# Kernel optimization log

Hardware: AMD Instinct MI355X
Metric: run time of the kernel (lower is better)

## Reference

```python
import jax, jax.numpy as jnp
import numpy as np

D_MODEL = 1024
QK_DIM = 1024
V_DIM = 1024
H = 16
TAU = 20.0
HQK = QK_DIM // H
HV = V_DIM // H
SCALE = HQK ** -0.5
SCALE_BASE = 512.0
EPS_GAMMA = 1e-8
EPS_GN = 1e-5


def _rotate_every_two(x):
    x1 = x[..., ::2]
    x2 = x[..., 1::2]
    return jnp.stack([-x2, x1], axis=-1).reshape(x.shape)


def _xpos_rotate(q, k, t):
    # q,k: (B,H,N,d); t: (B,N) continuous positions (timestamps in days)
    d = q.shape[-1]
    inv_freq = (1.0 / (10000.0 ** (np.arange(0, d, 2) / d))).astype(np.float32)  # (d/2,)
    sinusoid = t[:, None, :, None] * inv_freq  # (B,1,N,d/2)
    sin = jnp.repeat(jnp.sin(sinusoid), 2, axis=-1)  # (B,1,N,d)
    cos = jnp.repeat(jnp.cos(sinusoid), 2, axis=-1)
    scale_vec = ((np.arange(0, d, 2) + 0.4 * d) / (1.4 * d)).astype(np.float32)  # (d/2,)
    scale = jnp.repeat(scale_vec ** (t[:, None, :, None] / SCALE_BASE), 2, axis=-1)  # (B,1,N,d)
    q_rot = (q * cos + _rotate_every_two(q) * sin) * scale
    k_rot = (k * cos + _rotate_every_two(k) * sin) / scale
    return q_rot, k_rot


def setup_inputs() -> dict:
    key = jax.random.key(0)
    ks = jax.random.split(key, 6)
    B, N = 4, 1024
    X = jax.random.normal(ks[0], (B, N, D_MODEL), dtype=jnp.float32)
    # increasing timestamps in days
    timestamps = jnp.sort(jax.random.uniform(ks[1], (B, N), jnp.float32, 0.0, 100.0), axis=-1)
    W_qkv = jax.random.normal(ks[2], (D_MODEL, 2 * QK_DIM + V_DIM), dtype=jnp.float32) * 0.02
    W_gamma = jax.random.normal(ks[3], (D_MODEL, H), dtype=jnp.float32) * 0.02
    W_gated = jax.random.normal(ks[4], (D_MODEL, V_DIM), dtype=jnp.float32) * 0.02
    W_out = jax.random.normal(ks[5], (V_DIM, D_MODEL), dtype=jnp.float32) * 0.02
    return {"X": X, "timestamps": timestamps, "W_qkv": W_qkv, "W_gamma": W_gamma,
            "W_gated": W_gated, "W_out": W_out}


def reference(X, timestamps, W_qkv, W_gamma, W_gated, W_out):
    B, N, _ = X.shape
    qkv = X @ W_qkv  # (B,N,2*qk+v)
    q, k, v = jnp.split(qkv, [QK_DIM, 2 * QK_DIM], axis=-1)
    q = q.reshape(B, N, H, HQK).transpose(0, 2, 1, 3)  # (B,H,N,dk)
    k = k.reshape(B, N, H, HQK).transpose(0, 2, 1, 3)
    v = v.reshape(B, N, H, HV).transpose(0, 2, 1, 3)
    q, k = _xpos_rotate(q, k, timestamps)
    # data-dependent decay gamma in (0,1]
    gamma = jax.nn.sigmoid(X @ W_gamma) ** (1.0 / TAU)  # (B,N,H)
    log_b = jnp.cumsum(jnp.log(gamma + EPS_GAMMA), axis=1).transpose(0, 2, 1)  # (B,H,N)
    log_D = log_b[..., :, None] - log_b[..., None, :]  # (B,H,N,N)
    causal = jnp.tril(jnp.ones((N, N), dtype=bool))
    # masked_fill(-inf) then clamp[-80,0]: clip maps -inf -> -80 (matches torch)
    D = jnp.exp(jnp.clip(jnp.where(causal, log_D, -jnp.inf), -80.0, 0.0))
    attn = jnp.einsum('bhnd,bhmd->bhnm', q, k) * SCALE * D
    O = jnp.einsum('bhnm,bhmd->bhnd', attn, v)  # (B,H,N,dv)
    O = O.transpose(0, 2, 1, 3).reshape(B, N, V_DIM)
    # GroupNorm(num_groups=H, affine=False) over (channels-in-group, seq)
    g = O.reshape(B, N, H, HV)
    mu = g.mean(axis=(1, 3), keepdims=True)
    var = g.var(axis=(1, 3), keepdims=True)
    O = ((g - mu) / jnp.sqrt(var + EPS_GN)).reshape(B, N, V_DIM)
    O = jax.nn.silu(X @ W_gated) * O
    return O @ W_out
```

## Files before the change

### kernel.cpp

```cpp
#include <hip/hip_runtime.h>
#include <cstddef>
#include <cstdint>

#define NH 16
#define HD 64
#define NSEQ 1024
#define NB 4
#define DM 1024
#define SCALE 0.125f

typedef __attribute__((ext_vector_type(8))) short v8s;
typedef __attribute__((ext_vector_type(4))) float v4f;

__device__ __forceinline__ short f2bf(float x) {
    union { float f; unsigned u; } v; v.f = x;
    unsigned r = v.u + 0x7FFF + ((v.u >> 16) & 1);
    return (short)(r >> 16);
}
__device__ __forceinline__ float bf2f(short x) {
    union { unsigned u; float f; } v; v.u = ((unsigned)(unsigned short)x) << 16;
    return v.f;
}
__device__ __forceinline__ void gload16(const void* g, void* l) {
    __builtin_amdgcn_global_load_lds(
        (const __attribute__((address_space(1))) void*)g,
        (__attribute__((address_space(3))) void*)l, 16, 0, 0);
}
__device__ __forceinline__ int gswz(int r, int kbyte) {
    return (r * 64 + kbyte) ^ (((r >> 1) & 3) << 4);
}
__device__ __forceinline__ int aswz(int r, int byte) {
    return (r * 128 + byte) ^ ((r & 7) << 4);
}
#define SBAR() __builtin_amdgcn_s_barrier()
#define WAITV0() asm volatile("s_waitcnt vmcnt(0)" ::: "memory")
#define WAITV4() asm volatile("s_waitcnt vmcnt(4)" ::: "memory")
#define WAITL() asm volatile("s_waitcnt lgkmcnt(0)" ::: "memory")

__global__ __launch_bounds__(256) void convert_rows(const float* __restrict__ X,
                                                    short* __restrict__ Xb, int K) {
    const int kt = blockIdx.x, rt = blockIdx.y;
    const int t = threadIdx.x;
    const int rloc = t >> 1, kb0 = (t & 1) * 16;
    const float* src = X + (size_t)(rt * 128 + rloc) * K + kt * 32 + kb0;
    short o[16] __attribute__((aligned(16)));
#pragma unroll
    for (int j = 0; j < 16; j += 4) {
        float4 v = *(const float4*)(src + j);
        o[j] = f2bf(v.x); o[j + 1] = f2bf(v.y); o[j + 2] = f2bf(v.z); o[j + 3] = f2bf(v.w);
    }
    char* base = (char*)(Xb + ((size_t)rt * (K >> 5) + kt) * 4096);
#pragma unroll
    for (int c = 0; c < 2; ++c)
        *(v8s*)(base + gswz(rloc, kb0 * 2 + c * 16)) = *(v8s*)&o[c * 8];
}

__global__ __launch_bounds__(256) void tconv(const float* __restrict__ W,
                                             short* __restrict__ Bt,
                                             int K, int N) {
    __shared__ short lsm[32][136];
    const int ct = blockIdx.x, kt = blockIdx.y;
    const int t = threadIdx.x;
    {
        const int kk = t >> 3, nn0 = (t & 7) * 16;
        const float* src = W + (size_t)(kt * 32 + kk) * N + ct * 128 + nn0;
#pragma unroll
        for (int j = 0; j < 16; j += 4) {
            float4 v = *(const float4*)(src + j);
            lsm[kk][nn0 + j] = f2bf(v.x); lsm[kk][nn0 + j + 1] = f2bf(v.y);
            lsm[kk][nn0 + j + 2] = f2bf(v.z); lsm[kk][nn0 + j + 3] = f2bf(v.w);
        }
    }
    __syncthreads();
    const int rloc = t >> 1, kb0 = (t & 1) * 16;
    short o[16] __attribute__((aligned(16)));
#pragma unroll
    for (int j = 0; j < 16; ++j) o[j] = lsm[kb0 + j][rloc];
    char* base = (char*)(Bt + ((size_t)ct * (K >> 5) + kt) * 4096);
#pragma unroll
    for (int c = 0; c < 2; ++c)
        *(v8s*)(base + gswz(rloc, kb0 * 2 + c * 16)) = *(v8s*)&o[c * 8];
}

template<bool BF16OUT>
__global__ __launch_bounds__(256) void gemm_tt(const short* __restrict__ A,
                                               const short* __restrict__ B,
                                               void* __restrict__ C, int N) {
    __shared__ short As[4096];
    __shared__ short Bs[4096];
    const int tid = threadIdx.x;
    const int w = tid >> 6, l = tid & 63;
    const int wr = w >> 1, wc = w & 1;
    const int rt = blockIdx.y, ct = blockIdx.x;
    const char* Abase = (const char*)A + ((size_t)rt * 32) * 8192;
    const char* Bbase = (const char*)B + ((size_t)ct * 32) * 8192;

    v4f acc[4][4];
#pragma unroll
    for (int i = 0; i < 4; ++i)
#pragma unroll
        for (int j = 0; j < 4; ++j) acc[i][j] = (v4f){0.f, 0.f, 0.f, 0.f};

    for (int kt = 0; kt < 32; ++kt) {
        __syncthreads();
#pragma unroll
        for (int i = 0; i < 2; ++i) {
            const int c = w * 2 + i;
            gload16(Abase + (size_t)kt * 8192 + c * 1024 + l * 16, (char*)As + c * 1024);
            gload16(Bbase + (size_t)kt * 8192 + c * 1024 + l * 16, (char*)Bs + c * 1024);
        }
        __syncthreads();
        v8s af[4], bfr[4];
#pragma unroll
        for (int i = 0; i < 4; ++i) {
            const int ra = wr * 64 + i * 16 + (l & 15);
            af[i] = *(const v8s*)((char*)As + gswz(ra, (l >> 4) * 16));
            const int rb = wc * 64 + i * 16 + (l & 15);
            bfr[i] = *(const v8s*)((char*)Bs + gswz(rb, (l >> 4) * 16));
        }
#pragma unroll
        for (int i = 0; i < 4; ++i)
#pragma unroll
            for (int j = 0; j < 4; ++j)
                acc[i][j] = __builtin_amdgcn_mfma_f32_16x16x32_bf16(af[i], bfr[j], acc[i][j], 0, 0, 0);
    }
#pragma unroll
    for (int i = 0; i < 4; ++i)
#pragma unroll
        for (int j = 0; j < 4; ++j) {
            const int r0 = rt * 128 + wr * 64 + i * 16 + (l >> 4) * 4;
            const int cc = ct * 128 + wc * 64 + j * 16 + (l & 15);
#pragma unroll
            for (int t2 = 0; t2 < 4; ++t2) {
                if (BF16OUT) ((short*)C)[(size_t)(r0 + t2) * N + cc] = f2bf(acc[i][j][t2]);
                else         ((float*)C)[(size_t)(r0 + t2) * N + cc] = acc[i][j][t2];
            }
        }
}

__global__ __launch_bounds__(256) void gamma2(const float* __restrict__ X,
                                              const float* __restrict__ Wg,
                                              float* __restrict__ loggam) {
    __shared__ float wgs[1024 * 17];
    const int tid = threadIdx.x;
#pragma unroll
    for (int it = 0; it < 16; ++it) {
        const int idx = it * 1024 + tid * 4;
        float4 v = *(const float4*)(Wg + idx);
        const int k = idx >> 4, h0 = idx & 15;
        wgs[k * 17 + h0]     = v.x;
        wgs[k * 17 + h0 + 1] = v.y;
        wgs[k * 17 + h0 + 2] = v.z;
        wgs[k * 17 + h0 + 3] = v.w;
    }
    __syncthreads();

    const int r = tid >> 4, c = tid & 15;
    const int row = blockIdx.x * 16 + r;
    const float* xrow = X + (size_t)row * DM;
    float acc[16];
#pragma unroll
    for (int h = 0; h < 16; ++h) acc[h] = 0.0f;
#pragma unroll 4
    for (int i = 0; i < 16; ++i) {
        const int kb = i * 64 + c * 4;
        float4 xv = *(const float4*)(xrow + kb);
        const float xs[4] = {xv.x, xv.y, xv.z, xv.w};
#pragma unroll
        for (int j = 0; j < 4; ++j) {
            const float* wrow = &wgs[(kb + j) * 17];
#pragma unroll
            for (int h = 0; h < 16; ++h) acc[h] = fmaf(xs[j], wrow[h], acc[h]);
        }
    }
#pragma unroll
    for (int h = 0; h < 16; ++h) {
#pragma unroll
        for (int off = 8; off >= 1; off >>= 1)
            acc[h] += __shfl_xor(acc[h], off, 16);
    }
    const float d = acc[c];
    const float sig = 1.0f / (1.0f + expf(-d));
    const float gam = powf(sig, 1.0f / 20.0f);
    loggam[(size_t)row * NH + c] = logf(gam + 1e-8f);
}

__global__ __launch_bounds__(256) void scan_kernel(float* __restrict__ lg) {
    const int wave = threadIdx.x >> 6;
    const int lane = threadIdx.x & 63;
    const int bh = blockIdx.x * 4 + wave;
    const int b = bh >> 4, h = bh & 15;
    float* p = lg + (size_t)b * NSEQ * NH + h;
    const int n0 = lane * 16;
    float v[16];
    float s = 0.0f;
#pragma unroll
    for (int j = 0; j < 16; ++j) { v[j] = p[(size_t)(n0 + j) * NH]; s += v[j]; }
    float sc = s;
#pragma unroll
    for (int off = 1; off < 64; off <<= 1) {
        float o = __shfl_up(sc, off, 64);
        if (lane >= off) sc += o;
    }
    float acc = sc - s;
#pragma unroll
    for (int j = 0; j < 16; ++j) { acc += v[j]; p[(size_t)(n0 + j) * NH] = acc; }
}

__global__ __launch_bounds__(256) void prep(const short* __restrict__ qkvb,
                                            const float* __restrict__ ts,
                                            short* __restrict__ Qb,
                                            short* __restrict__ Kb,
                                            short* __restrict__ Vtb) {
    __shared__ short vsm[64][72];
    const int tile = blockIdx.x, bh = blockIdx.y;
    const int b = bh >> 4, h = bh & 15;
    const int t = threadIdx.x;
    const int rloc = t >> 2, d0 = (t & 3) * 16;
    const int row = b * NSEQ + tile * 64 + rloc;
    const short* src = qkvb + (size_t)row * 3072 + h * HD;
    const size_t tb = ((size_t)bh * 16 + tile) * 4096;

    float qa[16], ka[16];
    {
        v8s q0 = *(const v8s*)(src + d0), q1 = *(const v8s*)(src + d0 + 8);
        v8s k0 = *(const v8s*)(src + 1024 + d0), k1 = *(const v8s*)(src + 1024 + d0 + 8);
#pragma unroll
        for (int j = 0; j < 8; ++j) {
            qa[j] = bf2f(q0[j]); qa[j + 8] = bf2f(q1[j]);
            ka[j] = bf2f(k0[j]); ka[j + 8] = bf2f(k1[j]);
        }
    }
    const float tv = ts[row];
    short qo[16] __attribute__((aligned(16)));
    short ko[16] __attribute__((aligned(16)));
#pragma unroll
    for (int j = 0; j < 8; ++j) {
        const int i = (d0 >> 1) + j;
        const float inv_freq = exp2f(-0.4152410119f * (float)i);
        const float ang = tv * inv_freq;
        const float s = sinf(ang), c = cosf(ang);
        const float sv = ((float)(2 * i) + 25.6f) * (1.0f / 89.6f);
        const float e = log2f(sv) * tv * (1.0f / 512.0f);
        const float sc = exp2f(e) * SCALE, isc = exp2f(-e);
        qo[2 * j]     = f2bf((qa[2 * j] * c - qa[2 * j + 1] * s) * sc);
        qo[2 * j + 1] = f2bf((qa[2 * j + 1] * c + qa[2 * j] * s) * sc);
        ko[2 * j]     = f2bf((ka[2 * j] * c - ka[2 * j + 1] * s) * isc);
        ko[2 * j + 1] = f2bf((ka[2 * j + 1] * c + ka[2 * j] * s) * isc);
    }
#pragma unroll
    for (int c = 0; c < 2; ++c) {
        *(v8s*)((char*)(Qb + tb) + aswz(rloc, d0 * 2 + c * 16)) = *(v8s*)&qo[c * 8];
        *(v8s*)((char*)(Kb + tb) + aswz(rloc, d0 * 2 + c * 16)) = *(v8s*)&ko[c * 8];
    }
    {
        v8s v0 = *(const v8s*)(src + 2048 + d0), v1 = *(const v8s*)(src + 2048 + d0 + 8);
        *(short4*)&vsm[rloc][d0]      = *(short4*)&v0;
        *(short4*)&vsm[rloc][d0 + 4]  = *((short4*)&v0 + 1);
        *(short4*)&vsm[rloc][d0 + 8]  = *(short4*)&v1;
        *(short4*)&vsm[rloc][d0 + 12] = *((short4*)&v1 + 1);
    }
    __syncthreads();
    {
        const int d = t >> 2, m0 = (t & 3) * 16;
        short vt[16] __attribute__((aligned(16)));
#pragma unroll
        for (int j = 0; j < 16; ++j) vt[j] = vsm[m0 + j][d];
#pragma unroll
        for (int c = 0; c < 2; ++c)
            *(v8s*)((char*)(Vtb + tb) + aswz(d, m0 * 2 + c * 16)) = *(v8s*)&vt[c * 8];
    }
}

__global__ __launch_bounds__(256) void attn4(const short* __restrict__ Qb,
                                             const short* __restrict__ Kb,
                                             const short* __restrict__ Vtb,
                                             const float* __restrict__ logb,
                                             float* __restrict__ O,
                                             float* __restrict__ partial) {
    __shared__ short Ks[2][4096];
    __shared__ short Vts[2][4096];
    __shared__ short Ps[8192];
    __shared__ float lbAll[1024];
    __shared__ float emAll[1024];
    const int id = blockIdx.x;
    const int half = id >> 8;
    const int idx = id & 255;
    const int bh = ((idx & 7) << 3) | ((idx >> 3) & 7);
    const int qq = half == 0 ? (4 + (idx >> 6)) : (3 - (idx >> 6));
    const int b = bh >> 4, h = bh & 15;
    const int tid = threadIdx.x;
    const int w = tid >> 6, l = tid & 63;
    const int n0 = qq * 128;
    const int NT = 2 * qq + 2;

#pragma unroll
    for (int i = 0; i < 4; ++i) {
        const int c = w * 4 + i;
        gload16((const char*)Qb + ((size_t)bh * 16 + 2 * qq) * 8192 + c * 1024 + l * 16,
                (char*)Ps + c * 1024);
    }
    for (int i = tid; i < 1024; i += 256)
        lbAll[i] = logb[(size_t)(b * NSEQ + i) * NH + h];
    WAITV0(); WAITL();
    SBAR();

    const float base = lbAll[n0];
    for (int i = tid; i < NT * 64; i += 256) emAll[i] = __expf(base - lbAll[i]);
    float en[2][4];
#pragma unroll
    for (int rg = 0; rg < 2; ++rg)
#pragma unroll
        for (int t2 = 0; t2 < 4; ++t2)
            en[rg][t2] = __expf(lbAll[n0 + w * 32 + rg * 16 + (l >> 4) * 4 + t2] - base);
    v8s aq[2][2];
#pragma unroll
    for (int rg = 0; rg < 2; ++rg)
#pragma unroll
        for (int kc = 0; kc < 2; ++kc) {
            const int r = w * 32 + rg * 16 + (l & 15);
            aq[rg][kc] = *(const v8s*)((char*)Ps + (r >> 6) * 8192 +
                                       aswz(r & 63, kc * 64 + (l >> 4) * 16));
        }
    WAITL();
    SBAR();

    v4f oacc[2][4];
#pragma unroll
    for (int rg = 0; rg < 2; ++rg)
#pragma unroll
        for (int dt = 0; dt < 4; ++dt) oacc[rg][dt] = (v4f){0.f, 0.f, 0.f, 0.f};

#pragma unroll
    for (int i = 0; i < 2; ++i) {
        const int c = w * 2 + i;
        gload16((const char*)Kb + ((size_t)bh * 16 + 0) * 8192 + c * 1024 + l * 16,
                (char*)Ks + c * 1024);
        gload16((const char*)Vtb + ((size_t)bh * 16 + 0) * 8192 + c * 1024 + l * 16,
                (char*)Vts + c * 1024);
    }

    for (int t = 0; t < NT; ++t) {
        const int m0 = t * 64;
        const int buf = t & 1;
        SBAR();
        if (t + 1 < NT) {
            const int nb = (t + 1) & 1;
#pragma unroll
            for (int i = 0; i < 2; ++i) {
                const int c = w * 2 + i;
                gload16((const char*)Kb + ((size_t)bh * 16 + t + 1) * 8192 + c * 1024 + l * 16,
                        (char*)Ks + nb * 8192 + c * 1024);
                gload16((const char*)Vtb + ((size_t)bh * 16 + t + 1) * 8192 + c * 1024 + l * 16,
                        (char*)Vts + nb * 8192 + c * 1024);
            }
            WAITV4();
        } else {
            WAITV0();
        }
        SBAR();

        const bool active = (m0 <= n0 + w * 32 + 31);
        if (active) {
            const char* KsB = (const char*)Ks + buf * 8192;
            const char* VtsB = (const char*)Vts + buf * 8192;
            v4f sfr[2][4];
#pragma unroll
            for (int rg = 0; rg < 2; ++rg)
#pragma unroll
                for (int m4 = 0; m4 < 4; ++m4) sfr[rg][m4] = (v4f){0.f, 0.f, 0.f, 0.f};
#pragma unroll
            for (int m4 = 0; m4 < 4; ++m4) {
#pragma unroll
                for (int kc = 0; kc < 2; ++kc) {
                    const int m = m4 * 16 + (l & 15);
                    v8s bk = *(const v8s*)(KsB + aswz(m, kc * 64 + (l >> 4) * 16));
#pragma unroll
                    for (int rg = 0; rg < 2; ++rg)
                        sfr[rg][m4] = __builtin_amdgcn_mfma_f32_16x16x32_bf16(aq[rg][kc], bk, sfr[rg][m4], 0, 0, 0);
                }
            }
            const bool needMask = (m0 + 63) > (n0 + w * 32);
            float emv[4];
#pragma unroll
            for (int m4 = 0; m4 < 4; ++m4) emv[m4] = emAll[m0 + m4 * 16 + (l & 15)];
#pragma unroll
            for (int rg = 0; rg < 2; ++rg)
#pragma unroll
                for (int m4 = 0; m4 < 4; ++m4) {
                    const int m = m4 * 16 + (l & 15);
#pragma unroll
                    for (int t2 = 0; t2 < 4; ++t2) {
                        const int r = w * 32 + rg * 16 + (l >> 4) * 4 + t2;
                        float sval = sfr[rg][m4][t2] * en[rg][t2] * emv[m4];
                        if (needMask && (n0 + r) < (m0 + m)) sval = 0.0f;
                        *(short*)((char*)Ps + aswz(r, m * 2)) = f2bf(sval);
                    }
                }
            WAITL();
            __builtin_amdgcn_sched_barrier(0);
#pragma unroll
            for (int kc = 0; kc < 2; ++kc) {
                v8s ap[2];
#pragma unroll
                for (int rg = 0; rg < 2; ++rg) {
                    const int r = w * 32 + rg * 16 + (l & 15);
                    ap[rg] = *(const v8s*)((char*)Ps + aswz(r, kc * 64 + (l >> 4) * 16));
                }
#pragma unroll
                for (int dt = 0; dt < 4; ++dt) {
                    const int d = dt * 16 + (l & 15);
                    v8s bv = *(const v8s*)(VtsB + aswz(d, kc * 64 + (l >> 4) * 16));
#pragma unroll
                    for (int rg = 0; rg < 2; ++rg)
                        oacc[rg][dt] = __builtin_amdgcn_mfma_f32_16x16x32_bf16(ap[rg], bv, oacc[rg][dt], 0, 0, 0);
                }
            }
        }
    }
    float psum = 0.0f, pssq = 0.0f;
#pragma unroll
    for (int rg = 0; rg < 2; ++rg)
#pragma unroll
        for (int dt = 0; dt < 4; ++dt) {
            const int col = h * HD + dt * 16 + (l & 15);
            const int r0 = n0 + w * 32 + rg * 16 + (l >> 4) * 4;
#pragma unroll
            for (int t2 = 0; t2 < 4; ++t2) {
                const float v = oacc[rg][dt][t2];
                O[(size_t)(b * NSEQ + r0 + t2) * DM + col] = v;
                psum += v; pssq += v * v;
            }
        }
    __syncthreads();
    float* red = (float*)Ks;
    red[tid] = psum; red[256 + tid] = pssq;
    __syncthreads();
    for (int s = 128; s > 0; s >>= 1) {
        if (tid < s) { red[tid] += red[tid + s]; red[256 + tid] += red[256 + tid + s]; }
        __syncthreads();
    }
    if (tid == 0) {
        partial[(bh * 8 + qq) * 2]     = red[0];
        partial[(bh * 8 + qq) * 2 + 1] = red[256];
    }
}

__global__ __launch_bounds__(64) void gn_finalize(const float* __restrict__ partial,
                                                  float* __restrict__ stats) {
    const int bh = threadIdx.x;
    float s = 0.0f, q = 0.0f;
#pragma unroll
    for (int i = 0; i < 8; ++i) {
        s += partial[(bh * 8 + i) * 2];
        q += partial[(bh * 8 + i) * 2 + 1];
    }
    const float inv = 1.0f / (NSEQ * HD);
    const float mu = s * inv;
    const float var = q * inv - mu * mu;
    stats[bh * 2] = mu;
    stats[bh * 2 + 1] = rsqrtf(var + 1e-5f);
}

__global__ __launch_bounds__(256) void gate_kernel(const short* __restrict__ Gfb,
                                                   const float* __restrict__ O,
                                                   const float* __restrict__ stats,
                                                   short* __restrict__ Gb) {
    const size_t i4 = ((size_t)blockIdx.x * 256 + threadIdx.x) * 4;
    const int row = (int)(i4 >> 10);
    const int col = (int)(i4 & 1023);
    const int h = col >> 6;
    const int b = row >> 10;
    const float mu = stats[(b * NH + h) * 2];
    const float rstd = stats[(b * NH + h) * 2 + 1];
    short4 gv = *(const short4*)(Gfb + i4);
    float4 ov = *(const float4*)(O + i4);
    const float gs[4] = {bf2f(gv.x), bf2f(gv.y), bf2f(gv.z), bf2f(gv.w)};
    const float os[4] = {ov.x, ov.y, ov.z, ov.w};
    short o[4];
#pragma unroll
    for (int j = 0; j < 4; ++j) {
        const float g = gs[j];
        const float silu = g / (1.0f + __expf(-g));
        o[j] = f2bf(silu * (os[j] - mu) * rstd);
    }
    const int rt = row >> 7, rloc = row & 127;
    const int kt = col >> 5, kloc = col & 31;
    char* base = (char*)(Gb + ((size_t)rt * 32 + kt) * 4096);
    *(short4*)(base + gswz(rloc, kloc * 2)) = *(short4*)o;
}

extern "C" void kernel_launch(void* const* d_in, const int* in_sizes, int n_in,
                              void* d_out, int out_size, void* d_ws, size_t ws_size,
                              hipStream_t stream) {
    const float* X       = (const float*)d_in[0];
    const float* ts      = (const float*)d_in[1];
    const float* W_qkv   = (const float*)d_in[2];
    const float* W_gamma = (const float*)d_in[3];
    const float* W_gated = (const float*)d_in[4];
    const float* W_out   = (const float*)d_in[5];
    float* out = (float*)d_out;

    char* ws = (char*)d_ws;
    short* qkvb = (short*)ws;
    float* logb = (float*)(ws + 25165824);
    float* Oatt = (float*)(ws + 25427968);
    float* stats = (float*)(ws + 42205184);
    short* Xb   = (short*)(ws + 42205696);
    short* Wtq  = (short*)(ws + 50594304);
    short* Wtg  = (short*)(ws + 56885760);
    short* Wto  = (short*)(ws + 58982912);
    short* Qb   = (short*)(ws + 61080064);
    short* Kb   = (short*)(ws + 69468672);
    short* Vtb  = (short*)(ws + 77857280);
    short* Gfb  = qkvb;
    short* Gb   = Xb;
    float* partial = (float*)Wtq;

    convert_rows<<<dim3(32, 32), 256, 0, stream>>>(X, Xb, 1024);
    tconv<<<dim3(24, 32), 256, 0, stream>>>(W_qkv, Wtq, 1024, 3072);
    tconv<<<dim3(8, 32), 256, 0, stream>>>(W_gated, Wtg, 1024, 1024);
    tconv<<<dim3(8, 32), 256, 0, stream>>>(W_out, Wto, 1024, 1024);

    gemm_tt<true><<<dim3(24, 32), 256, 0, stream>>>(Xb, Wtq, qkvb, 3072);
    gamma2<<<256, 256, 0, stream>>>(X, W_gamma, logb);
    scan_kernel<<<16, 256, 0, stream>>>(logb);
    prep<<<dim3(16, 64), 256, 0, stream>>>(qkvb, ts, Qb, Kb, Vtb);
    attn4<<<512, 256, 0, stream>>>(Qb, Kb, Vtb, logb, Oatt, partial);
    gn_finalize<<<1, 64, 0, stream>>>(partial, stats);
    gemm_tt<true><<<dim3(8, 32), 256, 0, stream>>>(Xb, Wtg, Gfb, 1024);
    gate_kernel<<<4096, 256, 0, stream>>>(Gfb, Oatt, stats, Gb);
    gemm_tt<false><<<dim3(8, 32), 256, 0, stream>>>(Gb, Wto, out, 1024);
}
```

Measured before the change: 168.3 us.

## Fuse gating epilogue into gated GEMM and transpose attention MFMA outputs

Merges the SiLU gating and group-norm application into the epilogue of the gated GEMM, which removes the separate gate kernel and the bf16 round trip of the gate activations. The scan now writes log-decay in a transposed per-(batch,head) layout so attention loads it contiguously. In attention, the MFMA operands are swapped so each lane holds a row with consecutive columns, which allows vectorized P stores and float4 O stores. The new GEMM epilogue does scattered scalar reads of O and swizzled 2-byte writes, which may be less efficient than the old dedicated kernel.

```diff
diff --git a/kernel.cpp b/kernel.cpp
--- a/kernel.cpp
+++ b/kernel.cpp
@@ -82,10 +82,12 @@
         *(v8s*)(base + gswz(rloc, kb0 * 2 + c * 16)) = *(v8s*)&o[c * 8];
 }
 
-template<bool BF16OUT>
+template<int MODE>
 __global__ __launch_bounds__(256) void gemm_tt(const short* __restrict__ A,
                                                const short* __restrict__ B,
-                                               void* __restrict__ C, int N) {
+                                               void* __restrict__ C, int N,
+                                               const float* __restrict__ O,
+                                               const float* __restrict__ stats) {
     __shared__ short As[4096];
     __shared__ short Bs[4096];
     const int tid = threadIdx.x;
@@ -124,6 +126,12 @@
             for (int j = 0; j < 4; ++j)
                 acc[i][j] = __builtin_amdgcn_mfma_f32_16x16x32_bf16(af[i], bfr[j], acc[i][j], 0, 0, 0);
     }
+    float mu = 0.f, rstd = 0.f;
+    if (MODE == 2) {
+        const int hh = ct * 2 + wc;
+        mu   = stats[((rt >> 3) * NH + hh) * 2];
+        rstd = stats[((rt >> 3) * NH + hh) * 2 + 1];
+    }
 #pragma unroll
     for (int i = 0; i < 4; ++i)
 #pragma unroll
@@ -132,8 +140,18 @@
             const int cc = ct * 128 + wc * 64 + j * 16 + (l & 15);
 #pragma unroll
             for (int t2 = 0; t2 < 4; ++t2) {
-                if (BF16OUT) ((short*)C)[(size_t)(r0 + t2) * N + cc] = f2bf(acc[i][j][t2]);
-                else         ((float*)C)[(size_t)(r0 + t2) * N + cc] = acc[i][j][t2];
+                if (MODE == 1) ((short*)C)[(size_t)(r0 + t2) * N + cc] = f2bf(acc[i][j][t2]);
+                else if (MODE == 0) ((float*)C)[(size_t)(r0 + t2) * N + cc] = acc[i][j][t2];
+                else {
+                    const int row = r0 + t2;
+                    const float g = acc[i][j][t2];
+                    const float silu = g / (1.0f + __expf(-g));
+                    const float ov = O[(size_t)row * DM + cc];
+                    const float val = silu * (ov - mu) * rstd;
+                    const int rloc = row - rt * 128;
+                    char* base = (char*)((short*)C + ((size_t)rt * 32 + (cc >> 5)) * 4096);
+                    *(short*)(base + gswz(rloc, (cc & 31) * 2)) = f2bf(val);
+                }
             }
         }
 }
@@ -185,12 +203,13 @@
     loggam[(size_t)row * NH + c] = logf(gam + 1e-8f);
 }
 
-__global__ __launch_bounds__(256) void scan_kernel(float* __restrict__ lg) {
+__global__ __launch_bounds__(256) void scan_kernel(const float* __restrict__ lg,
+                                                   float* __restrict__ lgT) {
     const int wave = threadIdx.x >> 6;
     const int lane = threadIdx.x & 63;
     const int bh = blockIdx.x * 4 + wave;
     const int b = bh >> 4, h = bh & 15;
-    float* p = lg + (size_t)b * NSEQ * NH + h;
+    const float* p = lg + (size_t)b * NSEQ * NH + h;
     const int n0 = lane * 16;
     float v[16];
     float s = 0.0f;
@@ -203,8 +222,9 @@
         if (lane >= off) sc += o;
     }
     float acc = sc - s;
-#pragma unroll
-    for (int j = 0; j < 16; ++j) { acc += v[j]; p[(size_t)(n0 + j) * NH] = acc; }
+    float* q = lgT + (size_t)bh * NSEQ + n0;
+#pragma unroll
+    for (int j = 0; j < 16; ++j) { acc += v[j]; q[j] = acc; }
 }
 
 __global__ __launch_bounds__(256) void prep(const short* __restrict__ qkvb,
@@ -272,10 +292,10 @@
     }
 }
 
-__global__ __launch_bounds__(256) void attn4(const short* __restrict__ Qb,
+__global__ __launch_bounds__(256) void attn5(const short* __restrict__ Qb,
                                              const short* __restrict__ Kb,
                                              const short* __restrict__ Vtb,
-                                             const float* __restrict__ logb,
+                                             const float* __restrict__ logbT,
                                              float* __restrict__ O,
                                              float* __restrict__ partial) {
     __shared__ short Ks[2][4096];
@@ -301,18 +321,16 @@
                 (char*)Ps + c * 1024);
     }
     for (int i = tid; i < 1024; i += 256)
-        lbAll[i] = logb[(size_t)(b * NSEQ + i) * NH + h];
+        lbAll[i] = logbT[(size_t)bh * NSEQ + i];
     WAITV0(); WAITL();
     SBAR();
 
     const float base = lbAll[n0];
     for (int i = tid; i < NT * 64; i += 256) emAll[i] = __expf(base - lbAll[i]);
-    float en[2][4];
+    float en[2];
 #pragma unroll
     for (int rg = 0; rg < 2; ++rg)
-#pragma unroll
-        for (int t2 = 0; t2 < 4; ++t2)
-            en[rg][t2] = __expf(lbAll[n0 + w * 32 + rg * 16 + (l >> 4) * 4 + t2] - base);
+        en[rg] = __expf(lbAll[n0 + w * 32 + rg * 16 + (l & 15)] - base);
     v8s aq[2][2];
 #pragma unroll
     for (int rg = 0; rg < 2; ++rg)
@@ -377,26 +395,29 @@
                     v8s bk = *(const v8s*)(KsB + aswz(m, kc * 64 + (l >> 4) * 16));
 #pragma unroll
                     for (int rg = 0; rg < 2; ++rg)
-                        sfr[rg][m4] = __builtin_amdgcn_mfma_f32_16x16x32_bf16(aq[rg][kc], bk, sfr[rg][m4], 0, 0, 0);
+                        sfr[rg][m4] = __builtin_amdgcn_mfma_f32_16x16x32_bf16(bk, aq[rg][kc], sfr[rg][m4], 0, 0, 0);
                 }
             }
             const bool needMask = (m0 + 63) > (n0 + w * 32);
-            float emv[4];
-#pragma unroll
-            for (int m4 = 0; m4 < 4; ++m4) emv[m4] = emAll[m0 + m4 * 16 + (l & 15)];
-#pragma unroll
-            for (int rg = 0; rg < 2; ++rg)
+#pragma unroll
+            for (int rg = 0; rg < 2; ++rg) {
+                const int r = w * 32 + rg * 16 + (l & 15);
+                const float enr = en[rg];
 #pragma unroll
                 for (int m4 = 0; m4 < 4; ++m4) {
-                    const int m = m4 * 16 + (l & 15);
+                    const int mbase = m0 + m4 * 16 + (l >> 4) * 4;
+                    float4 emv = *(const float4*)&emAll[mbase];
+                    const float ems[4] = {emv.x, emv.y, emv.z, emv.w};
+                    union { short s[4]; uint2 u; } pk;
 #pragma unroll
                     for (int t2 = 0; t2 < 4; ++t2) {
-                        const int r = w * 32 + rg * 16 + (l >> 4) * 4 + t2;
-                        float sval = sfr[rg][m4][t2] * en[rg][t2] * emv[m4];
-                        if (needMask && (n0 + r) < (m0 + m)) sval = 0.0f;
-                        *(short*)((char*)Ps + aswz(r, m * 2)) = f2bf(sval);
+                        float sval = sfr[rg][m4][t2] * enr * ems[t2];
+                        if (needMask && (n0 + r) < (mbase + t2)) sval = 0.0f;
+                        pk.s[t2] = f2bf(sval);
                     }
+                    *(uint2*)((char*)Ps + aswz(r, (m4 * 16 + (l >> 4) * 4) * 2)) = pk.u;
                 }
+            }
             WAITL();
             __builtin_amdgcn_sched_barrier(0);
 #pragma unroll
@@ -413,25 +434,23 @@
                     v8s bv = *(const v8s*)(VtsB + aswz(d, kc * 64 + (l >> 4) * 16));
 #pragma unroll
                     for (int rg = 0; rg < 2; ++rg)
-                        oacc[rg][dt] = __builtin_amdgcn_mfma_f32_16x16x32_bf16(ap[rg], bv, oacc[rg][dt], 0, 0, 0);
+                        oacc[rg][dt] = __builtin_amdgcn_mfma_f32_16x16x32_bf16(bv, ap[rg], oacc[rg][dt], 0, 0, 0);
                 }
             }
         }
     }
     float psum = 0.0f, pssq = 0.0f;
 #pragma unroll
-    for (int rg = 0; rg < 2; ++rg)
+    for (int rg = 0; rg < 2; ++rg) {
+        const int row = n0 + w * 32 + rg * 16 + (l & 15);
 #pragma unroll
         for (int dt = 0; dt < 4; ++dt) {
-            const int col = h * HD + dt * 16 + (l & 15);
-            const int r0 = n0 + w * 32 + rg * 16 + (l >> 4) * 4;
-#pragma unroll
-            for (int t2 = 0; t2 < 4; ++t2) {
-                const float v = oacc[rg][dt][t2];
-                O[(size_t)(b * NSEQ + r0 + t2) * DM + col] = v;
-                psum += v; pssq += v * v;
-            }
-        }
+            const float4 v = {oacc[rg][dt][0], oacc[rg][dt][1], oacc[rg][dt][2], oacc[rg][dt][3]};
+            *(float4*)(O + (size_t)(b * NSEQ + row) * DM + h * HD + dt * 16 + (l >> 4) * 4) = v;
+            psum += v.x + v.y + v.z + v.w;
+            pssq += v.x * v.x + v.y * v.y + v.z * v.z + v.w * v.w;
+        }
+    }
     __syncthreads();
     float* red = (float*)Ks;
     red[tid] = psum; red[256 + tid] = pssq;
@@ -460,34 +479,6 @@
     const float var = q * inv - mu * mu;
     stats[bh * 2] = mu;
     stats[bh * 2 + 1] = rsqrtf(var + 1e-5f);
-}
-
-__global__ __launch_bounds__(256) void gate_kernel(const short* __restrict__ Gfb,
-                                                   const float* __restrict__ O,
-                                                   const float* __restrict__ stats,
-                                                   short* __restrict__ Gb) {
-    const size_t i4 = ((size_t)blockIdx.x * 256 + threadIdx.x) * 4;
-    const int row = (int)(i4 >> 10);
-    const int col = (int)(i4 & 1023);
-    const int h = col >> 6;
-    const int b = row >> 10;
-    const float mu = stats[(b * NH + h) * 2];
-    const float rstd = stats[(b * NH + h) * 2 + 1];
-    short4 gv = *(const short4*)(Gfb + i4);
-    float4 ov = *(const float4*)(O + i4);
-    const float gs[4] = {bf2f(gv.x), bf2f(gv.y), bf2f(gv.z), bf2f(gv.w)};
-    const float os[4] = {ov.x, ov.y, ov.z, ov.w};
-    short o[4];
-#pragma unroll
-    for (int j = 0; j < 4; ++j) {
-        const float g = gs[j];
-        const float silu = g / (1.0f + __expf(-g));
-        o[j] = f2bf(silu * (os[j] - mu) * rstd);
-    }
-    const int rt = row >> 7, rloc = row & 127;
-    const int kt = col >> 5, kloc = col & 31;
-    char* base = (char*)(Gb + ((size_t)rt * 32 + kt) * 4096);
-    *(short4*)(base + gswz(rloc, kloc * 2)) = *(short4*)o;
 }
 
 extern "C" void kernel_launch(void* const* d_in, const int* in_sizes, int n_in,
@@ -513,7 +504,7 @@
     short* Qb   = (short*)(ws + 61080064);
     short* Kb   = (short*)(ws + 69468672);
     short* Vtb  = (short*)(ws + 77857280);
-    short* Gfb  = qkvb;
+    float* logbT = (float*)(ws + 86245888);
     short* Gb   = Xb;
     float* partial = (float*)Wtq;
 
@@ -522,13 +513,12 @@
     tconv<<<dim3(8, 32), 256, 0, stream>>>(W_gated, Wtg, 1024, 1024);
     tconv<<<dim3(8, 32), 256, 0, stream>>>(W_out, Wto, 1024, 1024);
 
-    gemm_tt<true><<<dim3(24, 32), 256, 0, stream>>>(Xb, Wtq, qkvb, 3072);
+    gemm_tt<1><<<dim3(24, 32), 256, 0, stream>>>(Xb, Wtq, qkvb, 3072, nullptr, nullptr);
     gamma2<<<256, 256, 0, stream>>>(X, W_gamma, logb);
-    scan_kernel<<<16, 256, 0, stream>>>(logb);
+    scan_kernel<<<16, 256, 0, stream>>>(logb, logbT);
     prep<<<dim3(16, 64), 256, 0, stream>>>(qkvb, ts, Qb, Kb, Vtb);
-    attn4<<<512, 256, 0, stream>>>(Qb, Kb, Vtb, logb, Oatt, partial);
+    attn5<<<512, 256, 0, stream>>>(Qb, Kb, Vtb, logbT, Oatt, partial);
     gn_finalize<<<1, 64, 0, stream>>>(partial, stats);
-    gemm_tt<true><<<dim3(8, 32), 256, 0, stream>>>(Xb, Wtg, Gfb, 1024);
-    gate_kernel<<<4096, 256, 0, stream>>>(Gfb, Oatt, stats, Gb);
-    gemm_tt<false><<<dim3(8, 32), 256, 0, stream>>>(Gb, Wto, out, 1024);
-}
+    gemm_tt<2><<<dim3(8, 32), 256, 0, stream>>>(Xb, Wtg, Gb, 1024, Oatt, stats);
+    gemm_tt<0><<<dim3(8, 32), 256, 0, stream>>>(Gb, Wto, out, 1024, nullptr, nullptr);
+}
```

New measurement: 164.6 us. 2.2% less time.
